# Kernel tuning notes

Hardware: AMD Instinct MI355X
Metric: run time of the kernel (lower is better)

The kernel has to match this reference:

```python
import jax, jax.numpy as jnp
import numpy as np

B, C, H, W = 128, 512, 8, 64   # batch, featrue_layers, feature-map H/W
HID, EMB = 512, 512            # hidden_dim_de, embedding_size


def setup_inputs() -> dict:
    key = jax.random.key(0)
    ks = jax.random.split(key, 8)
    s_lin = 1.0 / np.sqrt(HID)
    s_conv = 1.0 / np.sqrt(C * 9)
    s_att = 1.0 / np.sqrt(EMB)
    return {
        "conv_f": jax.random.normal(ks[0], (B, C, H, W), jnp.float32),
        "h": jax.random.normal(ks[1], (B, HID), jnp.float32),
        "W_h": jax.random.uniform(ks[2], (EMB, HID), jnp.float32, -s_lin, s_lin),
        "b_h": jax.random.uniform(ks[3], (EMB,), jnp.float32, -s_lin, s_lin),
        "K_conv": jax.random.uniform(ks[4], (EMB, C, 3, 3), jnp.float32, -s_conv, s_conv),
        "b_conv": jax.random.uniform(ks[5], (EMB,), jnp.float32, -s_conv, s_conv),
        "w_att": jax.random.uniform(ks[6], (1, EMB), jnp.float32, -s_att, s_att),
        "b_att": jax.random.uniform(ks[7], (1,), jnp.float32, -s_att, s_att),
    }


def reference(conv_f, h, W_h, b_h, K_conv, b_conv, w_att, b_att):
    b, c, hh, ww = conv_f.shape
    L = hh * ww
    # g_em = Linear(h): [B, EMB], broadcast over L positions
    g_em = h @ W_h.T + b_h                                   # [B, EMB]
    # x_em = Conv2d(conv_f): [B, EMB, H, W] -> [B, L, EMB]
    x_em = jax.lax.conv_general_dilated(
        conv_f, K_conv, window_strides=(1, 1), padding="SAME",
        dimension_numbers=("NCHW", "OIHW", "NCHW"))
    x_em = x_em + b_conv[None, :, None, None]
    x_em = x_em.reshape(b, -1, L).transpose(0, 2, 1)         # [B, L, EMB]
    # additive attention scores (dropout = identity in eval mode)
    feat = jnp.tanh(x_em + g_em[:, None, :])                 # [B, L, EMB]
    e = feat @ w_att[0] + b_att[0]                           # [B, L]
    alpha = jax.nn.softmax(e, axis=-1)                       # [B, L]
    # weighted sum over positions of the ORIGINAL features
    org = conv_f.reshape(b, c, L)                            # [B, C, L]
    att_out = jnp.einsum("bl,bcl->bc", alpha, org)           # [B, C]
    return att_out, alpha
```

## Files before the change

### kernel.cpp

```cpp
#include <hip/hip_runtime.h>
#include <hip/hip_bf16.h>
#include <stdint.h>

#define B_ 128
#define C_ 512
#define H_ 8
#define W_ 64
#define L_ 512
#define EMB_ 512
#define HID_ 512
#define M_ 65536
#define PH 10
#define PW 66
#define PADSZ (B_*PH*PW*C_)
#define BT_SZ (9*EMB_*C_)
#define GEM_SZ (B_*EMB_)

typedef __attribute__((ext_vector_type(8))) short short8;
typedef __attribute__((ext_vector_type(4))) float f32x4;

__device__ __forceinline__ void gload16(const void* g, void* l) {
    __builtin_amdgcn_global_load_lds(
        (const __attribute__((address_space(1))) unsigned int*)g,
        (__attribute__((address_space(3))) unsigned int*)l, 16, 0, 0);
}

__global__ __launch_bounds__(256) void k_pad(const float* __restrict__ cf,
                                             __hip_bfloat16* __restrict__ pad) {
    int bid = blockIdx.x, t = threadIdx.x;
    int b = bid >> 3, y = bid & 7;
    for (int cc = 0; cc < 2; ++cc) {
        int c = cc * 256 + t;
        const float* src = cf + ((size_t)(b * C_ + c) * H_ + y) * W_;
        __hip_bfloat16* dst = pad + ((size_t)(b * PH + y + 1) * PW + 1) * C_ + c;
#pragma unroll
        for (int x = 0; x < W_; ++x)
            dst[(size_t)x * C_] = __float2bfloat16(src[x]);
    }
}

__global__ __launch_bounds__(256) void k_wt(const float* __restrict__ kc,
                                            __hip_bfloat16* __restrict__ bt) {
    int e = blockIdx.x, t = threadIdx.x;
    for (int cc = 0; cc < 2; ++cc) {
        int c = cc * 256 + t;
        const float* src = kc + (size_t)(e * C_ + c) * 9;
#pragma unroll
        for (int tap = 0; tap < 9; ++tap)
            bt[(size_t)tap * EMB_ * C_ + e * C_ + c] = __float2bfloat16(src[tap]);
    }
}

__global__ __launch_bounds__(256) void k_gem(const float* __restrict__ h,
                                             const float* __restrict__ Wh,
                                             const float* __restrict__ bh,
                                             float* __restrict__ gem) {
    int b = blockIdx.x, t = threadIdx.x;
    __shared__ float hs[HID_];
    hs[t] = h[b * HID_ + t];
    hs[t + 256] = h[b * HID_ + t + 256];
    __syncthreads();
    for (int e = t; e < EMB_; e += 256) {
        float acc = bh[e];
        const float4* wr = (const float4*)(Wh + (size_t)e * HID_);
#pragma unroll 4
        for (int k4 = 0; k4 < HID_ / 4; ++k4) {
            float4 w = wr[k4];
            const float* hp = &hs[k4 * 4];
            acc += w.x * hp[0] + w.y * hp[1] + w.z * hp[2] + w.w * hp[3];
        }
        gem[b * EMB_ + e] = acc;
    }
}

__global__ __launch_bounds__(256) void k_conv(const __hip_bfloat16* __restrict__ pad,
                                              const __hip_bfloat16* __restrict__ bt,
                                              const float* __restrict__ gem,
                                              const float* __restrict__ bconv,
                                              const float* __restrict__ watt,
                                              float* __restrict__ sp) {
    __shared__ __align__(16) char lds[32768];
    char* ldsA = lds;
    char* ldsB = lds + 16384;
    const int tid = threadIdx.x;
    const int lane = tid & 63, wid = tid >> 6;
    const int wm = wid >> 1, wn = wid & 1;
    int bid0 = blockIdx.x;
    int bid = (bid0 & 7) * 256 + (bid0 >> 3);
    const int tile_m = bid >> 2, tile_n = bid & 3;
    const int b = tile_m >> 2;

    int gA[4], gB[4];
#pragma unroll
    for (int i = 0; i < 4; ++i) {
        int s = i * 4096 + tid * 16;
        int row = s >> 7;
        int clocal = ((s & 127) ^ ((row & 7) << 4)) >> 1;
        int m = tile_m * 128 + row;
        int y = (m >> 6) & 7;
        int x = m & 63;
        gA[i] = ((b * PH + y) * PW + x) * C_ + clocal;
        int e = tile_n * 128 + row;
        gB[i] = e * C_ + clocal;
    }

    const int la = lane & 15, lg = lane >> 4;
    const int xorv = (lane & 7) << 4;
    const int cb0 = (lg * 16) ^ xorv;
    const int cb1 = (64 + lg * 16) ^ xorv;
    const char* Ard0 = ldsA + (wm * 64 + la) * 128 + cb0;
    const char* Ard1 = ldsA + (wm * 64 + la) * 128 + cb1;
    const char* Brd0 = ldsB + (wn * 64 + la) * 128 + cb0;
    const char* Brd1 = ldsB + (wn * 64 + la) * 128 + cb1;

    f32x4 acc[4][4];
#pragma unroll
    for (int i = 0; i < 4; ++i)
#pragma unroll
        for (int j = 0; j < 4; ++j)
            acc[i][j] = (f32x4){0.f, 0.f, 0.f, 0.f};

    for (int tap = 0; tap < 9; ++tap) {
        const int dy = tap / 3, dx = tap - dy * 3;
        const int aoff = (dy * PW + dx) * C_;
        const size_t boff = (size_t)tap * EMB_ * C_;
        for (int c0 = 0; c0 < C_; c0 += 64) {
#pragma unroll
            for (int i = 0; i < 4; ++i) {
                gload16(pad + gA[i] + aoff + c0, ldsA + i * 4096 + wid * 1024);
                gload16(bt + boff + gB[i] + c0, ldsB + i * 4096 + wid * 1024);
            }
            __syncthreads();
#pragma unroll
            for (int kk = 0; kk < 2; ++kk) {
                short8 af[4], bfr[4];
#pragma unroll
                for (int fm = 0; fm < 4; ++fm)
                    af[fm] = *(const short8*)((kk ? Ard1 : Ard0) + fm * 2048);
#pragma unroll
                for (int fn = 0; fn < 4; ++fn)
                    bfr[fn] = *(const short8*)((kk ? Brd1 : Brd0) + fn * 2048);
#pragma unroll
                for (int fm = 0; fm < 4; ++fm)
#pragma unroll
                    for (int fn = 0; fn < 4; ++fn)
                        acc[fm][fn] = __builtin_amdgcn_mfma_f32_16x16x32_bf16(
                            af[fm], bfr[fn], acc[fm][fn], 0, 0, 0);
            }
            __syncthreads();
        }
    }

    const int part = tile_n * 2 + wn;
    float addv[4], wv[4];
#pragma unroll
    for (int fn = 0; fn < 4; ++fn) {
        int e = tile_n * 128 + wn * 64 + fn * 16 + la;
        addv[fn] = bconv[e] + gem[b * EMB_ + e];
        wv[fn] = watt[e];
    }
#pragma unroll
    for (int fm = 0; fm < 4; ++fm) {
        float sj[4] = {0.f, 0.f, 0.f, 0.f};
#pragma unroll
        for (int fn = 0; fn < 4; ++fn)
#pragma unroll
            for (int j = 0; j < 4; ++j)
                sj[j] += tanhf(acc[fm][fn][j] + addv[fn]) * wv[fn];
#pragma unroll
        for (int mask = 1; mask < 16; mask <<= 1)
#pragma unroll
            for (int j = 0; j < 4; ++j)
                sj[j] += __shfl_xor(sj[j], mask, 64);
        if (la == 0) {
            int mrow = tile_m * 128 + wm * 64 + fm * 16 + lg * 4;
            *(float4*)(sp + (size_t)part * M_ + mrow) =
                make_float4(sj[0], sj[1], sj[2], sj[3]);
        }
    }
}

__global__ __launch_bounds__(512) void k_softmax(const float* __restrict__ sp,
                                                 const float* __restrict__ batt,
                                                 float* __restrict__ alpha) {
    int b = blockIdx.x, t = threadIdx.x;
    float s = batt[0];
#pragma unroll
    for (int p = 0; p < 8; ++p) s += sp[(size_t)p * M_ + b * L_ + t];
    int lane = t & 63, wid = t >> 6;
    __shared__ float red[8];
    float m = s;
#pragma unroll
    for (int mask = 1; mask < 64; mask <<= 1) m = fmaxf(m, __shfl_xor(m, mask, 64));
    if (lane == 0) red[wid] = m;
    __syncthreads();
    float M = red[0];
#pragma unroll
    for (int i = 1; i < 8; ++i) M = fmaxf(M, red[i]);
    float ev = __expf(s - M);
    float sum = ev;
#pragma unroll
    for (int mask = 1; mask < 64; mask <<= 1) sum += __shfl_xor(sum, mask, 64);
    __syncthreads();
    if (lane == 0) red[wid] = sum;
    __syncthreads();
    float S = 0.f;
#pragma unroll
    for (int i = 0; i < 8; ++i) S += red[i];
    alpha[b * L_ + t] = ev / S;
}

__global__ __launch_bounds__(256) void k_att(const float* __restrict__ cf,
                                             const float* __restrict__ alpha,
                                             float* __restrict__ att) {
    int bid = blockIdx.x;
    int b = bid >> 7, cg = bid & 127;
    int t = threadIdx.x, lane = t & 63, wid = t >> 6;
    int c = cg * 4 + wid;
    const float4* xr = (const float4*)(cf + (size_t)(b * C_ + c) * L_);
    const float4* ar = (const float4*)(alpha + b * L_);
    float acc = 0.f;
#pragma unroll
    for (int it = 0; it < 2; ++it) {
        float4 xv = xr[it * 64 + lane];
        float4 av = ar[it * 64 + lane];
        acc += xv.x * av.x + xv.y * av.y + xv.z * av.z + xv.w * av.w;
    }
#pragma unroll
    for (int mask = 1; mask < 64; mask <<= 1) acc += __shfl_xor(acc, mask, 64);
    if (lane == 0) att[b * C_ + c] = acc;
}

extern "C" void kernel_launch(void* const* d_in, const int* in_sizes, int n_in,
                              void* d_out, int out_size, void* d_ws, size_t ws_size,
                              hipStream_t stream) {
    const float* conv_f = (const float*)d_in[0];
    const float* h      = (const float*)d_in[1];
    const float* W_h    = (const float*)d_in[2];
    const float* b_h    = (const float*)d_in[3];
    const float* K_conv = (const float*)d_in[4];
    const float* b_conv = (const float*)d_in[5];
    const float* w_att  = (const float*)d_in[6];
    const float* b_att  = (const float*)d_in[7];
    float* out = (float*)d_out;

    char* ws = (char*)d_ws;
    __hip_bfloat16* pad = (__hip_bfloat16*)ws;
    __hip_bfloat16* bt  = (__hip_bfloat16*)(ws + (size_t)PADSZ * 2);
    float* gem = (float*)(ws + (size_t)PADSZ * 2 + (size_t)BT_SZ * 2);
    float* sp  = gem + GEM_SZ;

    hipMemsetAsync(pad, 0, (size_t)PADSZ * 2, stream);
    k_pad<<<B_ * H_, 256, 0, stream>>>(conv_f, pad);
    k_wt<<<EMB_, 256, 0, stream>>>(K_conv, bt);
    k_gem<<<B_, 256, 0, stream>>>(h, W_h, b_h, gem);
    k_conv<<<2048, 256, 0, stream>>>(pad, bt, gem, b_conv, w_att, sp);
    float* alpha = out + B_ * C_;
    k_softmax<<<B_, 512, 0, stream>>>(sp, b_att, alpha);
    k_att<<<B_ * C_ / 4, 256, 0, stream>>>(conv_f, alpha, out);
}
```

Before: 553.8 us.

## Enlarge conv GEMM tiles to 256x256 with double-buffered LDS prefetch pipeline

Rewrites the implicit-GEMM convolution kernel to use 256x256 tiles across 8 waves, with two 64 KB LDS buffers. Global-to-LDS loads for the next K-step are interleaved between MFMA groups, and a single barrier pair per step replaces the synchronous load-then-compute loop. It also raises MFMA priority with s_setprio and replaces tanhf with an exp-based fast tanh. The aim is to hide memory latency and improve operand reuse, at the cost of 128 KB of LDS per block, fewer blocks (512), and slightly lower tanh accuracy.

```diff
diff --git a/kernel.cpp b/kernel.cpp
--- a/kernel.cpp
+++ b/kernel.cpp
@@ -23,6 +23,12 @@
     __builtin_amdgcn_global_load_lds(
         (const __attribute__((address_space(1))) unsigned int*)g,
         (__attribute__((address_space(3))) unsigned int*)l, 16, 0, 0);
+}
+
+__device__ __forceinline__ float fast_tanh(float x) {
+    float e = __expf(2.0f * fabsf(x));
+    float r = 1.0f - __fdividef(2.0f, e + 1.0f);
+    return copysignf(r, x);
 }
 
 __global__ __launch_bounds__(256) void k_pad(const float* __restrict__ cf,
@@ -73,107 +79,141 @@
     }
 }
 
-__global__ __launch_bounds__(256) void k_conv(const __hip_bfloat16* __restrict__ pad,
-                                              const __hip_bfloat16* __restrict__ bt,
-                                              const float* __restrict__ gem,
-                                              const float* __restrict__ bconv,
-                                              const float* __restrict__ watt,
-                                              float* __restrict__ sp) {
-    __shared__ __align__(16) char lds[32768];
-    char* ldsA = lds;
-    char* ldsB = lds + 16384;
+#define MFMA16(a,b,c) __builtin_amdgcn_mfma_f32_16x16x32_bf16(a,b,c,0,0,0)
+
+__global__ __launch_bounds__(512, 2) void k_conv(const __hip_bfloat16* __restrict__ pad,
+                                                 const __hip_bfloat16* __restrict__ bt,
+                                                 const float* __restrict__ gem,
+                                                 const float* __restrict__ bconv,
+                                                 const float* __restrict__ watt,
+                                                 float* __restrict__ sp) {
+    __shared__ __align__(16) char lds[131072];
     const int tid = threadIdx.x;
     const int lane = tid & 63, wid = tid >> 6;
-    const int wm = wid >> 1, wn = wid & 1;
+    const int wm = wid >> 2, wn = wid & 3;
     int bid0 = blockIdx.x;
-    int bid = (bid0 & 7) * 256 + (bid0 >> 3);
-    const int tile_m = bid >> 2, tile_n = bid & 3;
-    const int b = tile_m >> 2;
+    int bid = (bid0 & 7) * 64 + (bid0 >> 3);
+    const int tile_m = bid >> 1, tile_n = bid & 1;
+    const int b = tile_m >> 1;
 
     int gA[4], gB[4];
 #pragma unroll
     for (int i = 0; i < 4; ++i) {
-        int s = i * 4096 + tid * 16;
+        int s = i * 8192 + tid * 16;
         int row = s >> 7;
         int clocal = ((s & 127) ^ ((row & 7) << 4)) >> 1;
-        int m = tile_m * 128 + row;
+        int m = tile_m * 256 + row;
         int y = (m >> 6) & 7;
         int x = m & 63;
         gA[i] = ((b * PH + y) * PW + x) * C_ + clocal;
-        int e = tile_n * 128 + row;
+        int e = tile_n * 256 + row;
         gB[i] = e * C_ + clocal;
     }
+    const int lsw = wid * 1024;
 
     const int la = lane & 15, lg = lane >> 4;
-    const int xorv = (lane & 7) << 4;
+    const int xorv = (la & 7) << 4;
     const int cb0 = (lg * 16) ^ xorv;
     const int cb1 = (64 + lg * 16) ^ xorv;
-    const char* Ard0 = ldsA + (wm * 64 + la) * 128 + cb0;
-    const char* Ard1 = ldsA + (wm * 64 + la) * 128 + cb1;
-    const char* Brd0 = ldsB + (wn * 64 + la) * 128 + cb0;
-    const char* Brd1 = ldsB + (wn * 64 + la) * 128 + cb1;
-
-    f32x4 acc[4][4];
-#pragma unroll
-    for (int i = 0; i < 4; ++i)
-#pragma unroll
-        for (int j = 0; j < 4; ++j)
-            acc[i][j] = (f32x4){0.f, 0.f, 0.f, 0.f};
-
-    for (int tap = 0; tap < 9; ++tap) {
-        const int dy = tap / 3, dx = tap - dy * 3;
-        const int aoff = (dy * PW + dx) * C_;
-        const size_t boff = (size_t)tap * EMB_ * C_;
-        for (int c0 = 0; c0 < C_; c0 += 64) {
-#pragma unroll
-            for (int i = 0; i < 4; ++i) {
-                gload16(pad + gA[i] + aoff + c0, ldsA + i * 4096 + wid * 1024);
-                gload16(bt + boff + gB[i] + c0, ldsB + i * 4096 + wid * 1024);
-            }
-            __syncthreads();
-#pragma unroll
-            for (int kk = 0; kk < 2; ++kk) {
-                short8 af[4], bfr[4];
-#pragma unroll
-                for (int fm = 0; fm < 4; ++fm)
-                    af[fm] = *(const short8*)((kk ? Ard1 : Ard0) + fm * 2048);
-#pragma unroll
-                for (int fn = 0; fn < 4; ++fn)
-                    bfr[fn] = *(const short8*)((kk ? Brd1 : Brd0) + fn * 2048);
-#pragma unroll
-                for (int fm = 0; fm < 4; ++fm)
-#pragma unroll
-                    for (int fn = 0; fn < 4; ++fn)
-                        acc[fm][fn] = __builtin_amdgcn_mfma_f32_16x16x32_bf16(
-                            af[fm], bfr[fn], acc[fm][fn], 0, 0, 0);
-            }
-            __syncthreads();
-        }
-    }
-
-    const int part = tile_n * 2 + wn;
+
+    f32x4 acc[8][4];
+#pragma unroll
+    for (int i = 0; i < 8; ++i)
+#pragma unroll
+        for (int j = 0; j < 4; ++j) acc[i][j] = (f32x4){0.f, 0.f, 0.f, 0.f};
+
+#define STAGE_A(i, nb, aofs) gload16(pad + gA[i] + (aofs), lds + (nb)*65536 + (i)*8192 + lsw)
+#define STAGE_B(i, nb, bofs) gload16(bt + gB[i] + (bofs), lds + (nb)*65536 + 32768 + (i)*8192 + lsw)
+
+    STAGE_A(0, 0, 0); STAGE_A(1, 0, 0); STAGE_A(2, 0, 0); STAGE_A(3, 0, 0);
+    STAGE_B(0, 0, 0); STAGE_B(1, 0, 0); STAGE_B(2, 0, 0); STAGE_B(3, 0, 0);
+
+    for (int kt = 0; kt < 72; ++kt) {
+        const int cur = kt & 1, nb = cur ^ 1;
+        const char* bufA = lds + cur * 65536;
+        const char* bufB = bufA + 32768;
+        const int ktn = (kt < 71) ? kt + 1 : 71;
+        const int tapn = ktn >> 3;
+        const int dyn_ = tapn / 3, dxn_ = tapn - dyn_ * 3;
+        const int aofsn = (dyn_ * PW + dxn_) * C_ + ((ktn & 7) << 6);
+        const int bofsn = tapn * (EMB_ * C_) + ((ktn & 7) << 6);
+
+        short8 af[8], bq0, bq1;
+        STAGE_A(0, nb, aofsn); STAGE_A(1, nb, aofsn);
+        asm volatile("s_waitcnt vmcnt(2)" ::: "memory");
+        __builtin_amdgcn_s_barrier();
+#pragma unroll
+        for (int fm = 0; fm < 8; ++fm)
+            af[fm] = *(const short8*)(bufA + (wm * 128 + fm * 16 + la) * 128 + cb0);
+        bq0 = *(const short8*)(bufB + (wn * 64 + la) * 128 + cb0);
+        bq1 = *(const short8*)(bufB + (wn * 64 + 16 + la) * 128 + cb0);
+        __builtin_amdgcn_s_setprio(1);
+#pragma unroll
+        for (int fm = 0; fm < 8; ++fm) {
+            acc[fm][0] = MFMA16(af[fm], bq0, acc[fm][0]);
+            acc[fm][1] = MFMA16(af[fm], bq1, acc[fm][1]);
+        }
+        __builtin_amdgcn_s_setprio(0);
+        STAGE_A(2, nb, aofsn); STAGE_A(3, nb, aofsn);
+        bq0 = *(const short8*)(bufB + (wn * 64 + 32 + la) * 128 + cb0);
+        bq1 = *(const short8*)(bufB + (wn * 64 + 48 + la) * 128 + cb0);
+        __builtin_amdgcn_s_setprio(1);
+#pragma unroll
+        for (int fm = 0; fm < 8; ++fm) {
+            acc[fm][2] = MFMA16(af[fm], bq0, acc[fm][2]);
+            acc[fm][3] = MFMA16(af[fm], bq1, acc[fm][3]);
+        }
+        __builtin_amdgcn_s_setprio(0);
+        STAGE_B(0, nb, bofsn); STAGE_B(1, nb, bofsn);
+#pragma unroll
+        for (int fm = 0; fm < 8; ++fm)
+            af[fm] = *(const short8*)(bufA + (wm * 128 + fm * 16 + la) * 128 + cb1);
+        bq0 = *(const short8*)(bufB + (wn * 64 + la) * 128 + cb1);
+        bq1 = *(const short8*)(bufB + (wn * 64 + 16 + la) * 128 + cb1);
+        __builtin_amdgcn_s_setprio(1);
+#pragma unroll
+        for (int fm = 0; fm < 8; ++fm) {
+            acc[fm][0] = MFMA16(af[fm], bq0, acc[fm][0]);
+            acc[fm][1] = MFMA16(af[fm], bq1, acc[fm][1]);
+        }
+        __builtin_amdgcn_s_setprio(0);
+        STAGE_B(2, nb, bofsn); STAGE_B(3, nb, bofsn);
+        bq0 = *(const short8*)(bufB + (wn * 64 + 32 + la) * 128 + cb1);
+        bq1 = *(const short8*)(bufB + (wn * 64 + 48 + la) * 128 + cb1);
+        __builtin_amdgcn_s_setprio(1);
+#pragma unroll
+        for (int fm = 0; fm < 8; ++fm) {
+            acc[fm][2] = MFMA16(af[fm], bq0, acc[fm][2]);
+            acc[fm][3] = MFMA16(af[fm], bq1, acc[fm][3]);
+        }
+        __builtin_amdgcn_s_setprio(0);
+        __builtin_amdgcn_s_barrier();
+    }
+    asm volatile("s_waitcnt vmcnt(0)" ::: "memory");
+
+    const int part = tile_n * 4 + wn;
     float addv[4], wv[4];
 #pragma unroll
     for (int fn = 0; fn < 4; ++fn) {
-        int e = tile_n * 128 + wn * 64 + fn * 16 + la;
+        int e = tile_n * 256 + wn * 64 + fn * 16 + la;
         addv[fn] = bconv[e] + gem[b * EMB_ + e];
         wv[fn] = watt[e];
     }
 #pragma unroll
-    for (int fm = 0; fm < 4; ++fm) {
+    for (int fm = 0; fm < 8; ++fm) {
         float sj[4] = {0.f, 0.f, 0.f, 0.f};
 #pragma unroll
         for (int fn = 0; fn < 4; ++fn)
 #pragma unroll
             for (int j = 0; j < 4; ++j)
-                sj[j] += tanhf(acc[fm][fn][j] + addv[fn]) * wv[fn];
+                sj[j] += fast_tanh(acc[fm][fn][j] + addv[fn]) * wv[fn];
 #pragma unroll
         for (int mask = 1; mask < 16; mask <<= 1)
 #pragma unroll
             for (int j = 0; j < 4; ++j)
                 sj[j] += __shfl_xor(sj[j], mask, 64);
         if (la == 0) {
-            int mrow = tile_m * 128 + wm * 64 + fm * 16 + lg * 4;
+            int mrow = tile_m * 256 + wm * 128 + fm * 16 + lg * 4;
             *(float4*)(sp + (size_t)part * M_ + mrow) =
                 make_float4(sj[0], sj[1], sj[2], sj[3]);
         }
@@ -254,7 +294,7 @@
     k_pad<<<B_ * H_, 256, 0, stream>>>(conv_f, pad);
     k_wt<<<EMB_, 256, 0, stream>>>(K_conv, bt);
     k_gem<<<B_, 256, 0, stream>>>(h, W_h, b_h, gem);
-    k_conv<<<2048, 256, 0, stream>>>(pad, bt, gem, b_conv, w_att, sp);
+    k_conv<<<512, 512, 0, stream>>>(pad, bt, gem, b_conv, w_att, sp);
     float* alpha = out + B_ * C_;
     k_softmax<<<B_, 512, 0, stream>>>(sp, b_att, alpha);
     k_att<<<B_ * C_ / 4, 256, 0, stream>>>(conv_f, alpha, out);
```

Measured after the change: 527.7 us. 1.05x faster.
